# Kernel optimization log

Measured on AMD Instinct MI355X. Metric: run time of the kernel, lower is better.

The kernel has to match this reference:

```python
import jax, jax.numpy as jnp
import numpy as np

B, L, W, S, STEPS, VOCAB, NLAB = 1024, 128, 512, 8, 12, 32, 10

def setup_inputs() -> dict:
    key = jax.random.key(0)
    ks = jax.random.split(key, 24)
    def nrm(k, shape, scale=0.05):
        return jax.random.normal(k, shape, jnp.float32) * scale
    x = jax.random.randint(ks[0], (B, L), 0, VOCAB)
    embed = nrm(ks[1], (VOCAB, W), 0.1).at[0].set(0.0)  # padding_idx=0
    return {
        'x': x,
        'embed': embed,
        'W_mix': nrm(ks[2], (W, 3 * W)), 'b_mix': jnp.zeros((W,), jnp.float32),
        'W_in': nrm(ks[3], (S, W, 2 * W)), 'b_in': jnp.zeros((S, W), jnp.float32),
        'W_link': nrm(ks[4], (S, W, W)), 'b_link': jnp.zeros((S, W), jnp.float32),
        'W_ih': nrm(ks[5], (S, 3 * W, W)), 'b_ih': jnp.zeros((S, 3 * W), jnp.float32),
        'W_hh': nrm(ks[6], (S, 3 * W, W)), 'b_hh': jnp.zeros((S, 3 * W), jnp.float32),
        'W_gate': nrm(ks[7], (S, 1, W)), 'b_gate': jnp.zeros((S, 1), jnp.float32),
        'phase': nrm(ks[8], (S, W), 0.5), 'prism_gain': jnp.zeros((S, W), jnp.float32),
        'W_delta': nrm(ks[9], (S, W, W)), 'b_delta': jnp.zeros((S, W), jnp.float32),
        'decay_param': jnp.zeros((), jnp.float32),
        'W_out': nrm(ks[10], (NLAB, W)), 'b_out': jnp.zeros((NLAB,), jnp.float32),
    }

def _encode(x, embed, W_mix, b_mix):
    emb = embed[x]                                          # [B,L,W]
    mask = (x != 0).astype(jnp.float32)[..., None]          # [B,L,1]
    summed = (emb * mask).sum(1)
    denom = jnp.maximum(mask.sum(1), 1.0)
    mean = summed / denom
    maxed = jnp.where(mask == 0, -10000.0, emb).max(1)
    maxed = jnp.where(jnp.isfinite(maxed), maxed, 0.0)
    last_idx = jnp.maximum(mask[..., 0].sum(1).astype(jnp.int32) - 1, 0)
    last = jnp.take_along_axis(emb, last_idx[:, None, None], axis=1)[:, 0]
    cat = jnp.concatenate([mean, maxed, last], -1)          # [B,3W]
    return jnp.tanh(cat @ W_mix.T + b_mix)

def _forward(x, embed, W_mix, b_mix, W_in, b_in, W_link, b_link, W_ih, b_ih,
             W_hh, b_hh, W_gate, b_gate, phase, prism_gain, W_delta, b_delta,
             decay_param, W_out, b_out):
    summary = _encode(x, embed, W_mix, b_mix)               # [B,W]
    decay = jax.nn.sigmoid(decay_param)
    inv_sqrt_s = np.float32(1.0 / np.sqrt(S))
    gain = jax.nn.softplus(prism_gain)[None]                # [1,S,W]

    def step(carry, _):
        h, hs = carry
        shared = jnp.concatenate([h, summary], -1)          # conditioned: [B,2W]
        f0 = jnp.tanh(jnp.einsum('swi,bi->bsw', W_in, shared) + b_in)      # [B,S,W]
        prev = jnp.roll(f0, 1, axis=1)                      # sparse ring: feats[(i-1)%S]
        feats = jnp.tanh(f0 + jnp.einsum('sow,bsw->bso', W_link, prev) + b_link)
        # recurrent side pockets: per-side GRUCell (torch gate order r,z,n)
        gi = jnp.einsum('sgw,bsw->bsg', W_ih, feats) + b_ih
        gh = jnp.einsum('sgw,bsw->bsg', W_hh, hs) + b_hh
        ir, iz, inn = jnp.split(gi, 3, -1)
        hr, hz, hn = jnp.split(gh, 3, -1)
        r = jax.nn.sigmoid(ir + hr)
        z = jax.nn.sigmoid(iz + hz)
        n = jnp.tanh(inn + r * hn)
        hs_new = (1.0 - z) * n + z * hs                     # [B,S,W]
        feat = hs_new
        gate = jax.nn.sigmoid(jnp.einsum('sow,bsw->bso', W_gate, feat) + b_gate)  # [B,S,1]
        feat = jnp.cos(feat + phase[None]) ** 2 * gain      # prismion
        upd = gate * jnp.tanh(jnp.einsum('sow,bsw->bso', W_delta, feat) + b_delta)
        delta = upd.sum(1) * inv_sqrt_s
        h_new = jnp.tanh(h * decay + delta)
        return (h_new, hs_new), None

    hs0 = jnp.zeros((B, S, W), jnp.float32)
    (h, _), _ = jax.lax.scan(step, (summary, hs0), None, length=STEPS)
    return h @ W_out.T + b_out                               # [B,10]

def reference(x, embed, W_mix, b_mix, W_in, b_in, W_link, b_link, W_ih, b_ih,
              W_hh, b_hh, W_gate, b_gate, phase, prism_gain, W_delta, b_delta,
              decay_param, W_out, b_out):
    return _forward(x, embed, W_mix, b_mix, W_in, b_in, W_link, b_link, W_ih,
                    b_ih, W_hh, b_hh, W_gate, b_gate, phase, prism_gain,
                    W_delta, b_delta, decay_param, W_out, b_out)
```

## Files before the change

### kernel.cpp

```cpp
#include <hip/hip_runtime.h>
#include <hip/hip_bf16.h>


typedef unsigned short u16;
typedef __attribute__((ext_vector_type(8))) short short8;
typedef __attribute__((ext_vector_type(4))) float f32x4;

__device__ __forceinline__ float bf2f(u16 v) {
    union { unsigned int u; float f; } x; x.u = ((unsigned int)v) << 16; return x.f;
}
__device__ __forceinline__ u16 f2bf(float f) {
    union { float f; unsigned int u; } x; x.f = f;
    unsigned int u = x.u;
    return (u16)((u + 0x7FFFu + ((u >> 16) & 1u)) >> 16);
}
__device__ __forceinline__ float fsig(float v) {
    return __builtin_amdgcn_rcpf(1.f + __expf(-v));
}
__device__ __forceinline__ float ftanh(float v) {
    return 1.f - 2.f * __builtin_amdgcn_rcpf(__expf(2.f * v) + 1.f);
}
__device__ __forceinline__ float fsoftplus(float v) {
    return (v > 20.f) ? v : __logf(1.f + __expf(v));
}

union U4 { ushort4 v; u16 e[4]; };

__device__ __forceinline__ void gload_lds16(const u16* g, u16* l) {
    __builtin_amdgcn_global_load_lds(
        (const __attribute__((address_space(1))) unsigned int*)g,
        (__attribute__((address_space(3))) unsigned int*)l, 16, 0, 0);
}

__device__ __forceinline__ int sane16(u16 u) {
    if ((u & 0x7FFF) == 0) return 1;
    int e = (u >> 7) & 0xFF;
    return (e >= 0x33 && e <= 0x43) ? 1 : 0;
}
__global__ __launch_bounds__(256) void detect_k(const u16* __restrict__ raw,
                                                int* __restrict__ flag) {
    const int t = threadIdx.x;
    int c = sane16(raw[1024 + t * 2]) + sane16(raw[1024 + t * 2 + 1]);
#pragma unroll
    for (int off = 32; off; off >>= 1) c += __shfl_down(c, off, 64);
    __shared__ int red[4];
    if ((t & 63) == 0) red[t >> 6] = c;
    __syncthreads();
    if (t == 0) *flag = (red[0] + red[1] + red[2] + red[3] >= 448) ? 1 : 0;
}

struct CT { const void* src[20]; int n[20]; int off[20]; };
__global__ __launch_bounds__(256) void conv_k(CT ct, u16* __restrict__ dstBase,
                                              const int* __restrict__ flag) {
    const int isbf = *flag;
    const int gid = blockIdx.x * 256 + threadIdx.x;
    const int stride = gridDim.x * 256;
    for (int tn = 0; tn < 20; ++tn) {
        const int n = ct.n[tn];
        const int n4 = n >> 2;
        u16* dst = dstBase + ct.off[tn];
        if (!isbf) {
            const float* s = (const float*)ct.src[tn];
            for (int i = gid; i < n4; i += stride) {
                f32x4 v = *(const f32x4*)(s + i * 4);
                *(ushort4*)(dst + i * 4) =
                    make_ushort4(f2bf(v[0]), f2bf(v[1]), f2bf(v[2]), f2bf(v[3]));
            }
            if (gid < (n & 3)) { int i = n4 * 4 + gid; dst[i] = f2bf(s[i]); }
        } else {
            const u16* s = (const u16*)ct.src[tn];
            for (int i = gid; i < n4; i += stride)
                *(ushort4*)(dst + i * 4) = *(const ushort4*)(s + i * 4);
            if (gid < (n & 3)) { int i = n4 * 4 + gid; dst[i] = s[i]; }
        }
    }
}

__global__ __launch_bounds__(256) void pack_k(const u16* __restrict__ Wih,
                                              const u16* __restrict__ Whh,
                                              u16* __restrict__ Wcat) {
    long i = ((long)blockIdx.x * 256 + threadIdx.x) * 8;
    if (i >= 8L * 1536 * 512) return;
    long sg = i >> 9;
    long k  = i & 511;
    *(short8*)(Wcat + sg * 1024 + k)       = *(const short8*)(Wih + i);
    *(short8*)(Wcat + sg * 1024 + 512 + k) = *(const short8*)(Whh + i);
}

struct GP {
    const u16* A;  long lda; long aOff[8];
    const u16* Bw; long ldb; long bwOff[8];
    const u16* bias; long biasOff[8];
    const u16* add; long ldadd; long addOff;
    const float* gate_pre;
    const u16* bgate;
    void* C; long ldc; long cOff[8];
    float* C2;
    u16* C3;
    int K; int nt;
};

template<int EPI, int MT>
__global__ __launch_bounds__(256) void gemm_k(GP p) {
    constexpr int MW   = MT / 32;
    constexpr int AITS = MT / 32;
    __shared__ __align__(16) u16 lA[2][MT * 64];
    __shared__ __align__(16) u16 lB[2][128 * 64];
    const int t    = threadIdx.x;
    const int lane = t & 63;
    const int wv   = t >> 6;
    const int bx   = blockIdx.x;
    const int z    = bx / p.nt;
    const int n0   = (bx - z * p.nt) * 128;
    const int m0   = blockIdx.y * MT;

    const u16* Ab = p.A + p.aOff[z] + (long)m0 * p.lda;
    const u16* Bb = p.Bw + p.bwOff[z] + (long)n0 * p.ldb;

    f32x4 acc[MW][4];
#pragma unroll
    for (int i = 0; i < MW; i++)
#pragma unroll
        for (int j = 0; j < 4; j++) acc[i][j] = (f32x4){0.f, 0.f, 0.f, 0.f};

    const int wm   = (wv & 1) * (MT / 2);
    const int wn   = (wv >> 1) * 64;
    const int fr   = lane & 15;
    const int quad = lane >> 4;

    const int nk = p.K >> 6;
#pragma unroll
    for (int it = 0; it < AITS; ++it) {
        int flat = it * 256 + t, row = flat >> 3, src = (flat & 7) ^ (row & 7);
        gload_lds16(Ab + (long)row * p.lda + src * 8, &lA[0][flat * 8]);
    }
#pragma unroll
    for (int it = 0; it < 4; ++it) {
        int flat = it * 256 + t, row = flat >> 3, src = (flat & 7) ^ (row & 7);
        gload_lds16(Bb + (long)row * p.ldb + src * 8, &lB[0][flat * 8]);
    }
    __syncthreads();

    for (int kt = 0; kt < nk; ++kt) {
        const int cur = kt & 1, nxt = cur ^ 1;
        if (kt + 1 < nk) {
            const long kb = (long)(kt + 1) * 64;
#pragma unroll
            for (int it = 0; it < AITS; ++it) {
                int flat = it * 256 + t, row = flat >> 3, src = (flat & 7) ^ (row & 7);
                gload_lds16(Ab + (long)row * p.lda + kb + src * 8, &lA[nxt][flat * 8]);
            }
#pragma unroll
            for (int it = 0; it < 4; ++it) {
                int flat = it * 256 + t, row = flat >> 3, src = (flat & 7) ^ (row & 7);
                gload_lds16(Bb + (long)row * p.ldb + kb + src * 8, &lB[nxt][flat * 8]);
            }
        }
#pragma unroll
        for (int kk = 0; kk < 2; ++kk) {
            const int q = kk * 4 + quad;
            short8 aF[MW], bF[4];
#pragma unroll
            for (int mi = 0; mi < MW; mi++) {
                int row = wm + mi * 16 + fr;
                aF[mi] = *(const short8*)&lA[cur][row * 64 + (q ^ (row & 7)) * 8];
            }
#pragma unroll
            for (int ni = 0; ni < 4; ni++) {
                int row = wn + ni * 16 + fr;
                bF[ni] = *(const short8*)&lB[cur][row * 64 + (q ^ (row & 7)) * 8];
            }
#pragma unroll
            for (int mi = 0; mi < MW; mi++)
#pragma unroll
                for (int ni = 0; ni < 4; ni++)
                    acc[mi][ni] = __builtin_amdgcn_mfma_f32_16x16x32_bf16(
                        aF[mi], bF[ni], acc[mi][ni], 0, 0, 0);
        }
        __syncthreads();
    }

    float sgv[MW][4];
    if (EPI == 3) {
#pragma unroll
        for (int mi = 0; mi < MW; mi++)
#pragma unroll
            for (int r = 0; r < 4; r++) {
                long row = m0 + wm + mi * 16 + quad * 4 + r;
                sgv[mi][r] = fsig(p.gate_pre[row * 8 + z] + bf2f(p.bgate[z]));
            }
    }

#pragma unroll
    for (int mi = 0; mi < MW; mi++) {
#pragma unroll
        for (int ni = 0; ni < 4; ni++) {
            const int mg = m0 + wm + mi * 16 + quad * 4;
            const int ng = n0 + wn + ni * 16 + fr;
#pragma unroll
            for (int r = 0; r < 4; r++) {
                float v = acc[mi][ni][r];
                const long row = mg + r;
                if (EPI == 1) {
                    float ad = bf2f(p.add[z * p.addOff + row * p.ldadd + ng]);
                    v = ftanh(v + ad + bf2f(p.bias[p.biasOff[z] + ng]));
                    ((u16*)p.C)[p.cOff[z] + row * p.ldc + ng] = f2bf(v);
                } else if (EPI == 3) {
                    v = ftanh(v + bf2f(p.bias[p.biasOff[z] + ng])) * sgv[mi][r];
                    ((u16*)p.C)[p.cOff[z] + row * p.ldc + ng] = f2bf(v);
                } else if (EPI == 4) {
                    v = ftanh(v + bf2f(p.bias[ng]));
                    u16 b = f2bf(v);
                    ((u16*)p.C)[row * 512 + ng] = b;
                    p.C3[row * 512 + ng] = b;
                    p.C2[row * 512 + ng] = v;
                } else if (EPI == 6) {
                    v = v + bf2f(p.bias[p.biasOff[z] + ng]);
                    ((u16*)p.C)[p.cOff[z] + row * p.ldc + ng] = f2bf(v);
                } else {
                    float ad = bf2f(p.add[row * p.ldadd + ng]);
                    v = ftanh(v + ad);
                    ((u16*)p.C)[row * p.ldc + ng] = f2bf(v);
                }
            }
        }
    }
}

struct GGP {
    const u16* fhs_in;
    u16* fhs_out;
    const u16* Wcat;
    const u16* b_ih;
    const u16* b_hh;
    u16* prism;
    float* gate_pre;
    const u16* Wg;
    const u16* phase;
    const u16* pgain;
};

__global__ __launch_bounds__(256, 2) void grug_k(GGP p) {
    __shared__ __align__(16) u16 sA[2][64 * 32];
    __shared__ __align__(16) u16 sW[2][3][128 * 32];
    const int t    = threadIdx.x;
    const int lane = t & 63;
    const int wv   = t >> 6;
    const int s    = blockIdx.x >> 2;
    const int w0   = (blockIdx.x & 3) * 128;
    const int m0   = blockIdx.y * 64;
    const int fr   = lane & 15;
    const int quad = lane >> 4;
    const int wn   = wv * 32;

    const u16* Ab = p.fhs_in + (long)m0 * 8192 + s * 1024;
    const u16* Wb = p.Wcat + (long)s * 1536 * 1024;

    f32x4 acc[4][4][2];
#pragma unroll
    for (int q = 0; q < 4; q++)
#pragma unroll
        for (int mi = 0; mi < 4; mi++)
#pragma unroll
            for (int ni = 0; ni < 2; ni++) acc[q][mi][ni] = (f32x4){0.f,0.f,0.f,0.f};

    const int arow = t >> 2, ac4 = t & 3, asrc = ac4 ^ ((arow >> 1) & 3);

    auto stageA = [&](int buf, long kb) {
        gload_lds16(Ab + (long)arow * 8192 + kb + asrc * 8, &sA[buf][t * 8]);
    };
    auto stageW = [&](int buf, long kb) {
#pragma unroll
        for (int q = 0; q < 3; q++)
#pragma unroll
            for (int it = 0; it < 2; ++it) {
                int flat = it * 256 + t, row = flat >> 2, src = (flat & 3) ^ ((row >> 1) & 3);
                long g = (long)(q * 512 + w0 + row);
                gload_lds16(Wb + g * 1024 + kb + src * 8, &sW[buf][q][flat * 8]);
            }
    };

    stageA(0, 0); stageW(0, 0);
    __syncthreads();

    for (int kt = 0; kt < 32; ++kt) {
        const int cur = kt & 1, nxt = cur ^ 1;
        if (kt + 1 < 32) { stageA(nxt, (long)(kt + 1) * 32); stageW(nxt, (long)(kt + 1) * 32); }
        const int qsel = (kt < 16) ? 2 : 3;
        short8 aF[4], bF[3][2];
#pragma unroll
        for (int mi = 0; mi < 4; mi++) {
            int row = mi * 16 + fr;
            aF[mi] = *(const short8*)&sA[cur][row * 32 + ((quad ^ ((row >> 1) & 3)) & 3) * 8];
        }
#pragma unroll
        for (int q = 0; q < 3; q++)
#pragma unroll
            for (int ni = 0; ni < 2; ni++) {
                int row = wn + ni * 16 + fr;
                bF[q][ni] = *(const short8*)&sW[cur][q][row * 32 + ((quad ^ ((row >> 1) & 3)) & 3) * 8];
            }
#pragma unroll
        for (int mi = 0; mi < 4; mi++)
#pragma unroll
            for (int ni = 0; ni < 2; ni++) {
                acc[0][mi][ni] = __builtin_amdgcn_mfma_f32_16x16x32_bf16(aF[mi], bF[0][ni], acc[0][mi][ni], 0, 0, 0);
                acc[1][mi][ni] = __builtin_amdgcn_mfma_f32_16x16x32_bf16(aF[mi], bF[1][ni], acc[1][mi][ni], 0, 0, 0);
                if (qsel == 2)
                    acc[2][mi][ni] = __builtin_amdgcn_mfma_f32_16x16x32_bf16(aF[mi], bF[2][ni], acc[2][mi][ni], 0, 0, 0);
                else
                    acc[3][mi][ni] = __builtin_amdgcn_mfma_f32_16x16x32_bf16(aF[mi], bF[2][ni], acc[3][mi][ni], 0, 0, 0);
            }
        __syncthreads();
    }

    const u16* bih = p.b_ih + (long)s * 1536;
    const u16* bhh = p.b_hh + (long)s * 1536;
    float gp[4][4];
#pragma unroll
    for (int mi = 0; mi < 4; mi++)
#pragma unroll
        for (int r = 0; r < 4; r++) gp[mi][r] = 0.f;

#pragma unroll
    for (int ni = 0; ni < 2; ni++) {
        const int col = w0 + wn + ni * 16 + fr;
        const float br  = bf2f(bih[col])        + bf2f(bhh[col]);
        const float bz  = bf2f(bih[512 + col])  + bf2f(bhh[512 + col]);
        const float bin = bf2f(bih[1024 + col]);
        const float bhn = bf2f(bhh[1024 + col]);
        const float ph  = bf2f(p.phase[s * 512 + col]);
        const float gain = fsoftplus(bf2f(p.pgain[s * 512 + col]));
        const float wg  = bf2f(p.Wg[s * 512 + col]);
#pragma unroll
        for (int mi = 0; mi < 4; mi++) {
#pragma unroll
            for (int r = 0; r < 4; r++) {
                const long b = m0 + mi * 16 + quad * 4 + r;
                float rv = fsig(acc[0][mi][ni][r] + br);
                float zv = fsig(acc[1][mi][ni][r] + bz);
                float nv = ftanh(acc[2][mi][ni][r] + bin + rv * (acc[3][mi][ni][r] + bhn));
                float hold = bf2f(p.fhs_in[b * 8192 + s * 1024 + 512 + col]);
                float hv = (1.f - zv) * nv + zv * hold;
                p.fhs_out[b * 8192 + s * 1024 + 512 + col] = f2bf(hv);
                float c = __cosf(hv + ph);
                p.prism[b * 4096 + s * 512 + col] = f2bf(c * c * gain);
                gp[mi][r] += wg * hv;
            }
        }
    }
#pragma unroll
    for (int m = 1; m < 16; m <<= 1)
#pragma unroll
        for (int mi = 0; mi < 4; mi++)
#pragma unroll
            for (int r = 0; r < 4; r++) gp[mi][r] += __shfl_xor(gp[mi][r], m, 64);
    if (fr == 0) {
#pragma unroll
        for (int mi = 0; mi < 4; mi++)
#pragma unroll
            for (int r = 0; r < 4; r++) {
                long b = m0 + mi * 16 + quad * 4 + r;
                atomicAdd(&p.gate_pre[b * 8 + s], gp[mi][r]);
            }
    }
}

__global__ __launch_bounds__(256) void encode_k(const int* __restrict__ x,
                                                const u16* __restrict__ embed,
                                                u16* __restrict__ cat) {
    __shared__ int toks[128];
    __shared__ int cnt_s;
    const int b = blockIdx.x, t = threadIdx.x;
    if (t < 128) toks[t] = x[b * 128 + t];
    __syncthreads();
    if (t == 0) {
        int c = 0;
        for (int l = 0; l < 128; l++) c += (toks[l] != 0);
        cnt_s = c;
    }
    __syncthreads();
    const int cnt = cnt_s;
    const int lastTok = toks[cnt > 0 ? cnt - 1 : 0];
    for (int w = t; w < 512; w += 256) {
        float sum = 0.f, mx = -10000.f;
        for (int l = 0; l < 128; l++) {
            int tok = toks[l];
            if (tok != 0) {
                float e = bf2f(embed[tok * 512 + w]);
                sum += e;
                mx = fmaxf(mx, e);
            }
        }
        float mean = sum / (float)(cnt > 0 ? cnt : 1);
        float last = bf2f(embed[lastTok * 512 + w]);
        cat[(long)b * 1536 + w]        = f2bf(mean);
        cat[(long)b * 1536 + 512 + w]  = f2bf(mx);
        cat[(long)b * 1536 + 1024 + w] = f2bf(last);
    }
}

__global__ __launch_bounds__(256) void hupd_k(const u16* __restrict__ upd,
                                              float* __restrict__ h,
                                              u16* __restrict__ h_b,
                                              const u16* __restrict__ decay_p) {
    const int idx = blockIdx.x * 256 + threadIdx.x;
    const int b = idx >> 9, w = idx & 511;
    const long base = (long)b * 4096 + w;
    float dsum = 0.f;
#pragma unroll
    for (int s = 0; s < 8; s++) dsum += bf2f(upd[base + s * 512]);
    const float decay = fsig(bf2f(decay_p[0]));
    const float hv = ftanh(h[idx] * decay + dsum * 0.35355339059327373f);
    h[idx] = hv;
    h_b[idx] = f2bf(hv);
}

__global__ __launch_bounds__(64) void out_k(const float* __restrict__ h,
                                            const u16* __restrict__ Wout,
                                            const u16* __restrict__ bout,
                                            void* __restrict__ out,
                                            const int* __restrict__ flag) {
    const int b = blockIdx.x, lane = threadIdx.x;
    const int isbf = *flag;
    for (int j = 0; j < 10; j++) {
        float p = 0.f;
#pragma unroll
        for (int k = 0; k < 8; k++) {
            int w = lane + k * 64;
            p += h[(long)b * 512 + w] * bf2f(Wout[j * 512 + w]);
        }
#pragma unroll
        for (int off = 32; off; off >>= 1) p += __shfl_down(p, off, 64);
        if (lane == 0) {
            float val = p + bf2f(bout[j]);
            if (isbf) ((u16*)out)[b * 10 + j] = f2bf(val);
            else      ((float*)out)[b * 10 + j] = val;
        }
    }
}

extern "C" void kernel_launch(void* const* d_in, const int* in_sizes, int n_in,
                              void* d_out, int out_size, void* d_ws, size_t ws_size,
                              hipStream_t stream) {
    (void)n_in; (void)out_size; (void)ws_size;
    const int* x = (const int*)d_in[0];

    char* pp = (char*)d_ws;
    auto carve = [&](size_t n) { char* r = pp; pp += (n + 255) & ~(size_t)255; return (void*)r; };

    CT ct;
    size_t ctot = 0;
    for (int i = 0; i < 20; i++) {
        ct.src[i] = d_in[i + 1];
        ct.n[i]   = in_sizes[i + 1];
        ct.off[i] = (int)ctot;
        ctot += ((size_t)in_sizes[i + 1] + 15) & ~(size_t)15;
    }
    u16* canon = (u16*)carve(ctot * 2);
    const u16* embed  = canon + ct.off[0];
    const u16* W_mix  = canon + ct.off[1];
    const u16* b_mix  = canon + ct.off[2];
    const u16* W_in   = canon + ct.off[3];
    const u16* b_in   = canon + ct.off[4];
    const u16* W_link = canon + ct.off[5];
    const u16* b_link = canon + ct.off[6];
    const u16* W_ih   = canon + ct.off[7];
    const u16* b_ih   = canon + ct.off[8];
    const u16* W_hh   = canon + ct.off[9];
    const u16* b_hh   = canon + ct.off[10];
    const u16* W_gate = canon + ct.off[11];
    const u16* b_gate = canon + ct.off[12];
    const u16* phase  = canon + ct.off[13];
    const u16* pgain  = canon + ct.off[14];
    const u16* W_delta= canon + ct.off[15];
    const u16* b_delta= canon + ct.off[16];
    const u16* decayp = canon + ct.off[17];
    const u16* W_out  = canon + ct.off[18];
    const u16* b_out  = canon + ct.off[19];

    int*   flag   = (int*)  carve(256);
    u16*   Wcat   = (u16*)  carve((size_t)8 * 1536 * 1024 * 2);
    u16*   cat    = (u16*)  carve((size_t)1024 * 1536 * 2);
    u16*   h_b    = (u16*)  carve((size_t)1024 * 512 * 2);
    u16*   summ_b = (u16*)  carve((size_t)1024 * 512 * 2);
    float* h      = (float*)carve((size_t)1024 * 512 * 4);
    u16*   cin    = (u16*)  carve((size_t)1024 * 4096 * 2);
    u16*   f0     = (u16*)  carve((size_t)1024 * 4096 * 2);
    u16*   fhs0   = (u16*)  carve((size_t)1024 * 8192 * 2);
    u16*   fhs1   = (u16*)  carve((size_t)1024 * 8192 * 2);
    u16*   prism  = (u16*)  carve((size_t)1024 * 4096 * 2);
    u16*   upd    = (u16*)  carve((size_t)1024 * 4096 * 2);
    float* gate_pre = (float*)carve((size_t)1024 * 8 * 4);

    (void)hipMemsetAsync(fhs0, 0, (size_t)1024 * 8192 * 2, stream);
    (void)hipMemsetAsync(fhs1, 0, (size_t)1024 * 8192 * 2, stream);

    detect_k<<<dim3(1), dim3(256), 0, stream>>>((const u16*)d_in[1], flag);
    conv_k<<<dim3(1024), dim3(256), 0, stream>>>(ct, canon, flag);
    pack_k<<<dim3(3072), dim3(256), 0, stream>>>(W_ih, W_hh, Wcat);
    encode_k<<<dim3(1024), dim3(256), 0, stream>>>(x, embed, cat);

    {
        GP p{}; p.A = cat; p.lda = 1536; p.Bw = W_mix; p.ldb = 1536;
        p.bias = b_mix; p.C = h_b; p.ldc = 512; p.C2 = h; p.C3 = summ_b;
        p.K = 1536; p.nt = 4;
        gemm_k<4, 64><<<dim3(4, 16, 1), dim3(256), 0, stream>>>(p);
    }
    {
        GP p{}; p.A = summ_b; p.lda = 512; p.Bw = W_in + 512; p.ldb = 1024;
        p.bias = b_in; p.C = cin; p.ldc = 4096; p.K = 512; p.nt = 32;
        gemm_k<6, 64><<<dim3(32, 16, 1), dim3(256), 0, stream>>>(p);
    }

    for (int step = 0; step < 12; ++step) {
        u16* fhs_cur = (step & 1) ? fhs1 : fhs0;
        u16* fhs_nxt = (step & 1) ? fhs0 : fhs1;
        {
            GP p{}; p.A = h_b; p.lda = 512; p.Bw = W_in; p.ldb = 1024;
            p.add = cin; p.ldadd = 4096; p.C = f0; p.ldc = 4096;
            p.K = 512; p.nt = 32;
            gemm_k<7, 64><<<dim3(32, 16, 1), dim3(256), 0, stream>>>(p);
        }
        {
            GP p{}; p.A = f0; p.lda = 4096;
            for (int s = 0; s < 8; s++) p.aOff[s] = (long)((s + 7) & 7) * 512;
            p.Bw = W_link; p.ldb = 512;
            for (int s = 0; s < 8; s++) p.bwOff[s] = (long)s * 512 * 512;
            p.bias = b_link;
            for (int s = 0; s < 8; s++) p.biasOff[s] = (long)s * 512;
            p.add = f0; p.ldadd = 4096; p.addOff = 512;
            p.C = fhs_cur; p.ldc = 8192;
            for (int s = 0; s < 8; s++) p.cOff[s] = (long)s * 1024;
            p.K = 512; p.nt = 4;
            gemm_k<1, 64><<<dim3(32, 16, 1), dim3(256), 0, stream>>>(p);
        }
        (void)hipMemsetAsync(gate_pre, 0, (size_t)1024 * 8 * 4, stream);
        {
            GGP g{};
            g.fhs_in = fhs_cur; g.fhs_out = fhs_nxt; g.Wcat = Wcat;
            g.b_ih = b_ih; g.b_hh = b_hh; g.prism = prism; g.gate_pre = gate_pre;
            g.Wg = W_gate; g.phase = phase; g.pgain = pgain;
            grug_k<<<dim3(32, 16, 1), dim3(256), 0, stream>>>(g);
        }
        {
            GP p{}; p.A = prism; p.lda = 4096;
            for (int s = 0; s < 8; s++) p.aOff[s] = (long)s * 512;
            p.Bw = W_delta; p.ldb = 512;
            for (int s = 0; s < 8; s++) p.bwOff[s] = (long)s * 512 * 512;
            p.bias = b_delta;
            for (int s = 0; s < 8; s++) p.biasOff[s] = (long)s * 512;
            p.gate_pre = gate_pre; p.bgate = b_gate;
            p.C = upd; p.ldc = 4096;
            for (int s = 0; s < 8; s++) p.cOff[s] = (long)s * 512;
            p.K = 512; p.nt = 4;
            gemm_k<3, 64><<<dim3(32, 16, 1), dim3(256), 0, stream>>>(p);
        }
        hupd_k<<<dim3(2048), dim3(256), 0, stream>>>(upd, h, h_b, decayp);
    }

    out_k<<<dim3(1024), dim3(64), 0, stream>>>(h, W_out, b_out, d_out, flag);
}
```

Measured before the change: 1.536 ms.

## Fuse delta GEMM, gating and hidden update into one kernel; retile GRU kernel

The per-slot W_delta GEMM, the sigmoid gating, the sum over slots and the hidden-state tanh update now run in a single kernel (updh_k). Each block loops over all 8 slots and accumulates the gated tanh outputs in registers, so the bf16 upd intermediate and the separate hupd_k launch go away. Separately, grug_k is retiled to 64-column blocks, which doubles the grid and shrinks per-thread accumulators and LDS. The fused kernel launches only 64 blocks with a long serial K loop, which may leave many compute units idle.

```diff
diff --git a/kernel.cpp b/kernel.cpp
--- a/kernel.cpp
+++ b/kernel.cpp
@@ -92,8 +92,6 @@
     const u16* Bw; long ldb; long bwOff[8];
     const u16* bias; long biasOff[8];
     const u16* add; long ldadd; long addOff;
-    const float* gate_pre;
-    const u16* bgate;
     void* C; long ldc; long cOff[8];
     float* C2;
     u16* C3;
@@ -180,17 +178,6 @@
         __syncthreads();
     }
 
-    float sgv[MW][4];
-    if (EPI == 3) {
-#pragma unroll
-        for (int mi = 0; mi < MW; mi++)
-#pragma unroll
-            for (int r = 0; r < 4; r++) {
-                long row = m0 + wm + mi * 16 + quad * 4 + r;
-                sgv[mi][r] = fsig(p.gate_pre[row * 8 + z] + bf2f(p.bgate[z]));
-            }
-    }
-
 #pragma unroll
     for (int mi = 0; mi < MW; mi++) {
 #pragma unroll
@@ -204,9 +191,6 @@
                 if (EPI == 1) {
                     float ad = bf2f(p.add[z * p.addOff + row * p.ldadd + ng]);
                     v = ftanh(v + ad + bf2f(p.bias[p.biasOff[z] + ng]));
-                    ((u16*)p.C)[p.cOff[z] + row * p.ldc + ng] = f2bf(v);
-                } else if (EPI == 3) {
-                    v = ftanh(v + bf2f(p.bias[p.biasOff[z] + ng])) * sgv[mi][r];
                     ((u16*)p.C)[p.cOff[z] + row * p.ldc + ng] = f2bf(v);
                 } else if (EPI == 4) {
                     v = ftanh(v + bf2f(p.bias[ng]));
@@ -240,44 +224,39 @@
     const u16* pgain;
 };
 
-__global__ __launch_bounds__(256, 2) void grug_k(GGP p) {
+__global__ __launch_bounds__(256) void grug_k(GGP p) {
     __shared__ __align__(16) u16 sA[2][64 * 32];
-    __shared__ __align__(16) u16 sW[2][3][128 * 32];
+    __shared__ __align__(16) u16 sW[2][3][64 * 32];
     const int t    = threadIdx.x;
     const int lane = t & 63;
     const int wv   = t >> 6;
-    const int s    = blockIdx.x >> 2;
-    const int w0   = (blockIdx.x & 3) * 128;
+    const int s    = blockIdx.x >> 3;
+    const int w0   = (blockIdx.x & 7) * 64;
     const int m0   = blockIdx.y * 64;
     const int fr   = lane & 15;
     const int quad = lane >> 4;
-    const int wn   = wv * 32;
+    const int wn   = wv * 16;
 
     const u16* Ab = p.fhs_in + (long)m0 * 8192 + s * 1024;
     const u16* Wb = p.Wcat + (long)s * 1536 * 1024;
 
-    f32x4 acc[4][4][2];
+    f32x4 acc[4][4];
 #pragma unroll
     for (int q = 0; q < 4; q++)
 #pragma unroll
-        for (int mi = 0; mi < 4; mi++)
-#pragma unroll
-            for (int ni = 0; ni < 2; ni++) acc[q][mi][ni] = (f32x4){0.f,0.f,0.f,0.f};
-
-    const int arow = t >> 2, ac4 = t & 3, asrc = ac4 ^ ((arow >> 1) & 3);
+        for (int mi = 0; mi < 4; mi++) acc[q][mi] = (f32x4){0.f,0.f,0.f,0.f};
+
+    const int arow = t >> 2, asrc = (t & 3) ^ ((arow >> 1) & 3);
 
     auto stageA = [&](int buf, long kb) {
         gload_lds16(Ab + (long)arow * 8192 + kb + asrc * 8, &sA[buf][t * 8]);
     };
     auto stageW = [&](int buf, long kb) {
 #pragma unroll
-        for (int q = 0; q < 3; q++)
-#pragma unroll
-            for (int it = 0; it < 2; ++it) {
-                int flat = it * 256 + t, row = flat >> 2, src = (flat & 3) ^ ((row >> 1) & 3);
-                long g = (long)(q * 512 + w0 + row);
-                gload_lds16(Wb + g * 1024 + kb + src * 8, &sW[buf][q][flat * 8]);
-            }
+        for (int q = 0; q < 3; q++) {
+            long g = (long)(q * 512 + w0 + arow);
+            gload_lds16(Wb + g * 1024 + kb + asrc * 8, &sW[buf][q][t * 8]);
+        }
     };
 
     stageA(0, 0); stageW(0, 0);
@@ -287,66 +266,57 @@
         const int cur = kt & 1, nxt = cur ^ 1;
         if (kt + 1 < 32) { stageA(nxt, (long)(kt + 1) * 32); stageW(nxt, (long)(kt + 1) * 32); }
         const int qsel = (kt < 16) ? 2 : 3;
-        short8 aF[4], bF[3][2];
+        short8 aF[4], bFq[3];
 #pragma unroll
         for (int mi = 0; mi < 4; mi++) {
             int row = mi * 16 + fr;
             aF[mi] = *(const short8*)&sA[cur][row * 32 + ((quad ^ ((row >> 1) & 3)) & 3) * 8];
         }
-#pragma unroll
-        for (int q = 0; q < 3; q++)
-#pragma unroll
-            for (int ni = 0; ni < 2; ni++) {
-                int row = wn + ni * 16 + fr;
-                bF[q][ni] = *(const short8*)&sW[cur][q][row * 32 + ((quad ^ ((row >> 1) & 3)) & 3) * 8];
-            }
-#pragma unroll
-        for (int mi = 0; mi < 4; mi++)
-#pragma unroll
-            for (int ni = 0; ni < 2; ni++) {
-                acc[0][mi][ni] = __builtin_amdgcn_mfma_f32_16x16x32_bf16(aF[mi], bF[0][ni], acc[0][mi][ni], 0, 0, 0);
-                acc[1][mi][ni] = __builtin_amdgcn_mfma_f32_16x16x32_bf16(aF[mi], bF[1][ni], acc[1][mi][ni], 0, 0, 0);
-                if (qsel == 2)
-                    acc[2][mi][ni] = __builtin_amdgcn_mfma_f32_16x16x32_bf16(aF[mi], bF[2][ni], acc[2][mi][ni], 0, 0, 0);
-                else
-                    acc[3][mi][ni] = __builtin_amdgcn_mfma_f32_16x16x32_bf16(aF[mi], bF[2][ni], acc[3][mi][ni], 0, 0, 0);
-            }
+        {
+            int row = wn + fr;
+            int sw = ((quad ^ ((row >> 1) & 3)) & 3) * 8;
+#pragma unroll
+            for (int q = 0; q < 3; q++)
+                bFq[q] = *(const short8*)&sW[cur][q][row * 32 + sw];
+        }
+#pragma unroll
+        for (int mi = 0; mi < 4; mi++) {
+            acc[0][mi] = __builtin_amdgcn_mfma_f32_16x16x32_bf16(aF[mi], bFq[0], acc[0][mi], 0, 0, 0);
+            acc[1][mi] = __builtin_amdgcn_mfma_f32_16x16x32_bf16(aF[mi], bFq[1], acc[1][mi], 0, 0, 0);
+            if (qsel == 2)
+                acc[2][mi] = __builtin_amdgcn_mfma_f32_16x16x32_bf16(aF[mi], bFq[2], acc[2][mi], 0, 0, 0);
+            else
+                acc[3][mi] = __builtin_amdgcn_mfma_f32_16x16x32_bf16(aF[mi], bFq[2], acc[3][mi], 0, 0, 0);
+        }
         __syncthreads();
     }
 
     const u16* bih = p.b_ih + (long)s * 1536;
     const u16* bhh = p.b_hh + (long)s * 1536;
+    const int col = w0 + wn + fr;
+    const float br  = bf2f(bih[col])        + bf2f(bhh[col]);
+    const float bz  = bf2f(bih[512 + col])  + bf2f(bhh[512 + col]);
+    const float bin = bf2f(bih[1024 + col]);
+    const float bhn = bf2f(bhh[1024 + col]);
+    const float ph  = bf2f(p.phase[s * 512 + col]);
+    const float gain = fsoftplus(bf2f(p.pgain[s * 512 + col]));
+    const float wg  = bf2f(p.Wg[s * 512 + col]);
+
     float gp[4][4];
 #pragma unroll
-    for (int mi = 0; mi < 4; mi++)
-#pragma unroll
-        for (int r = 0; r < 4; r++) gp[mi][r] = 0.f;
-
-#pragma unroll
-    for (int ni = 0; ni < 2; ni++) {
-        const int col = w0 + wn + ni * 16 + fr;
-        const float br  = bf2f(bih[col])        + bf2f(bhh[col]);
-        const float bz  = bf2f(bih[512 + col])  + bf2f(bhh[512 + col]);
-        const float bin = bf2f(bih[1024 + col]);
-        const float bhn = bf2f(bhh[1024 + col]);
-        const float ph  = bf2f(p.phase[s * 512 + col]);
-        const float gain = fsoftplus(bf2f(p.pgain[s * 512 + col]));
-        const float wg  = bf2f(p.Wg[s * 512 + col]);
-#pragma unroll
-        for (int mi = 0; mi < 4; mi++) {
-#pragma unroll
-            for (int r = 0; r < 4; r++) {
-                const long b = m0 + mi * 16 + quad * 4 + r;
-                float rv = fsig(acc[0][mi][ni][r] + br);
-                float zv = fsig(acc[1][mi][ni][r] + bz);
-                float nv = ftanh(acc[2][mi][ni][r] + bin + rv * (acc[3][mi][ni][r] + bhn));
-                float hold = bf2f(p.fhs_in[b * 8192 + s * 1024 + 512 + col]);
-                float hv = (1.f - zv) * nv + zv * hold;
-                p.fhs_out[b * 8192 + s * 1024 + 512 + col] = f2bf(hv);
-                float c = __cosf(hv + ph);
-                p.prism[b * 4096 + s * 512 + col] = f2bf(c * c * gain);
-                gp[mi][r] += wg * hv;
-            }
+    for (int mi = 0; mi < 4; mi++) {
+#pragma unroll
+        for (int r = 0; r < 4; r++) {
+            const long b = m0 + mi * 16 + quad * 4 + r;
+            float rv = fsig(acc[0][mi][r] + br);
+            float zv = fsig(acc[1][mi][r] + bz);
+            float nv = ftanh(acc[2][mi][r] + bin + rv * (acc[3][mi][r] + bhn));
+            float hold = bf2f(p.fhs_in[b * 8192 + s * 1024 + 512 + col]);
+            float hv = (1.f - zv) * nv + zv * hold;
+            p.fhs_out[b * 8192 + s * 1024 + 512 + col] = f2bf(hv);
+            float c = __cosf(hv + ph);
+            p.prism[b * 4096 + s * 512 + col] = f2bf(c * c * gain);
+            gp[mi][r] = wg * hv;
         }
     }
 #pragma unroll
@@ -364,6 +334,126 @@
                 atomicAdd(&p.gate_pre[b * 8 + s], gp[mi][r]);
             }
     }
+}
+
+struct UP {
+    const u16* prism;
+    const u16* Wd;
+    const u16* bd;
+    const float* gate_pre;
+    const u16* bgate;
+    float* h; u16* h_b;
+    const u16* decayp;
+};
+
+__global__ __launch_bounds__(256) void updh_k(UP p) {
+    __shared__ __align__(16) u16 lA[2][64 * 64];
+    __shared__ __align__(16) u16 lB[2][128 * 64];
+    const int t    = threadIdx.x;
+    const int lane = t & 63;
+    const int wv   = t >> 6;
+    const int n0   = blockIdx.x * 128;
+    const int m0   = blockIdx.y * 64;
+    const int wm   = (wv & 1) * 32;
+    const int wn   = (wv >> 1) * 64;
+    const int fr   = lane & 15;
+    const int quad = lane >> 4;
+
+    f32x4 acc[2][4], dsum[2][4];
+#pragma unroll
+    for (int i = 0; i < 2; i++)
+#pragma unroll
+        for (int j = 0; j < 4; j++) { acc[i][j] = (f32x4){0.f,0.f,0.f,0.f}; dsum[i][j] = (f32x4){0.f,0.f,0.f,0.f}; }
+
+    auto stageA = [&](int buf, int z, long kb) {
+        const u16* Ab = p.prism + (long)m0 * 4096 + z * 512;
+#pragma unroll
+        for (int it = 0; it < 2; ++it) {
+            int flat = it * 256 + t, row = flat >> 3, src = (flat & 7) ^ (row & 7);
+            gload_lds16(Ab + (long)row * 4096 + kb + src * 8, &lA[buf][flat * 8]);
+        }
+    };
+    auto stageB = [&](int buf, int z, long kb) {
+        const u16* Bb = p.Wd + (long)z * 512 * 512 + (long)n0 * 512;
+#pragma unroll
+        for (int it = 0; it < 4; ++it) {
+            int flat = it * 256 + t, row = flat >> 3, src = (flat & 7) ^ (row & 7);
+            gload_lds16(Bb + (long)row * 512 + kb + src * 8, &lB[buf][flat * 8]);
+        }
+    };
+
+    stageA(0, 0, 0); stageB(0, 0, 0);
+    __syncthreads();
+    const float decay = fsig(bf2f(p.decayp[0]));
+
+    for (int g = 0; g < 64; ++g) {
+        const int cur = g & 1, nxt = cur ^ 1;
+        if (g + 1 < 64) {
+            int z2 = (g + 1) >> 3; long k2 = (long)((g + 1) & 7) * 64;
+            stageA(nxt, z2, k2); stageB(nxt, z2, k2);
+        }
+#pragma unroll
+        for (int kk = 0; kk < 2; ++kk) {
+            const int q = kk * 4 + quad;
+            short8 aF[2], bF[4];
+#pragma unroll
+            for (int mi = 0; mi < 2; mi++) {
+                int row = wm + mi * 16 + fr;
+                aF[mi] = *(const short8*)&lA[cur][row * 64 + (q ^ (row & 7)) * 8];
+            }
+#pragma unroll
+            for (int ni = 0; ni < 4; ni++) {
+                int row = wn + ni * 16 + fr;
+                bF[ni] = *(const short8*)&lB[cur][row * 64 + (q ^ (row & 7)) * 8];
+            }
+#pragma unroll
+            for (int mi = 0; mi < 2; mi++)
+#pragma unroll
+                for (int ni = 0; ni < 4; ni++)
+                    acc[mi][ni] = __builtin_amdgcn_mfma_f32_16x16x32_bf16(
+                        aF[mi], bF[ni], acc[mi][ni], 0, 0, 0);
+        }
+        if ((g & 7) == 7) {
+            const int z = g >> 3;
+            const float bgz = bf2f(p.bgate[z]);
+            float sg[2][4];
+#pragma unroll
+            for (int mi = 0; mi < 2; mi++)
+#pragma unroll
+                for (int r = 0; r < 4; r++) {
+                    long row = m0 + wm + mi * 16 + quad * 4 + r;
+                    sg[mi][r] = fsig(p.gate_pre[row * 8 + z] + bgz);
+                }
+#pragma unroll
+            for (int ni = 0; ni < 4; ni++) {
+                const int col = n0 + wn + ni * 16 + fr;
+                const float bdz = bf2f(p.bd[z * 512 + col]);
+#pragma unroll
+                for (int mi = 0; mi < 2; mi++)
+#pragma unroll
+                    for (int r = 0; r < 4; r++) {
+                        dsum[mi][ni][r] += ftanh(acc[mi][ni][r] + bdz) * sg[mi][r];
+                        acc[mi][ni][r] = 0.f;
+                    }
+            }
+        }
+        __syncthreads();
+    }
+
+#pragma unroll
+    for (int mi = 0; mi < 2; mi++)
+#pragma unroll
+        for (int ni = 0; ni < 4; ni++) {
+            const int col = n0 + wn + ni * 16 + fr;
+#pragma unroll
+            for (int r = 0; r < 4; r++) {
+                long row = m0 + wm + mi * 16 + quad * 4 + r;
+                long idx = row * 512 + col;
+                float hv = ftanh(p.h[idx] * decay + dsum[mi][ni][r] * 0.35355339059327373f);
+                p.h[idx] = hv;
+                p.h_b[idx] = f2bf(hv);
+            }
+        }
 }
 
 __global__ __launch_bounds__(256) void encode_k(const int* __restrict__ x,
@@ -398,22 +488,6 @@
         cat[(long)b * 1536 + 512 + w]  = f2bf(mx);
         cat[(long)b * 1536 + 1024 + w] = f2bf(last);
     }
-}
-
-__global__ __launch_bounds__(256) void hupd_k(const u16* __restrict__ upd,
-                                              float* __restrict__ h,
-                                              u16* __restrict__ h_b,
-                                              const u16* __restrict__ decay_p) {
-    const int idx = blockIdx.x * 256 + threadIdx.x;
-    const int b = idx >> 9, w = idx & 511;
-    const long base = (long)b * 4096 + w;
-    float dsum = 0.f;
-#pragma unroll
-    for (int s = 0; s < 8; s++) dsum += bf2f(upd[base + s * 512]);
-    const float decay = fsig(bf2f(decay_p[0]));
-    const float hv = ftanh(h[idx] * decay + dsum * 0.35355339059327373f);
-    h[idx] = hv;
-    h_b[idx] = f2bf(hv);
 }
 
 __global__ __launch_bounds__(64) void out_k(const float* __restrict__ h,
@@ -490,7 +564,6 @@
     u16*   fhs0   = (u16*)  carve((size_t)1024 * 8192 * 2);
     u16*   fhs1   = (u16*)  carve((size_t)1024 * 8192 * 2);
     u16*   prism  = (u16*)  carve((size_t)1024 * 4096 * 2);
-    u16*   upd    = (u16*)  carve((size_t)1024 * 4096 * 2);
     float* gate_pre = (float*)carve((size_t)1024 * 8 * 4);
 
     (void)hipMemsetAsync(fhs0, 0, (size_t)1024 * 8192 * 2, stream);
@@ -541,22 +614,15 @@
             g.fhs_in = fhs_cur; g.fhs_out = fhs_nxt; g.Wcat = Wcat;
             g.b_ih = b_ih; g.b_hh = b_hh; g.prism = prism; g.gate_pre = gate_pre;
             g.Wg = W_gate; g.phase = phase; g.pgain = pgain;
-            grug_k<<<dim3(32, 16, 1), dim3(256), 0, stream>>>(g);
+            grug_k<<<dim3(64, 16, 1), dim3(256), 0, stream>>>(g);
         }
         {
-            GP p{}; p.A = prism; p.lda = 4096;
-            for (int s = 0; s < 8; s++) p.aOff[s] = (long)s * 512;
-            p.Bw = W_delta; p.ldb = 512;
-            for (int s = 0; s < 8; s++) p.bwOff[s] = (long)s * 512 * 512;
-            p.bias = b_delta;
-            for (int s = 0; s < 8; s++) p.biasOff[s] = (long)s * 512;
-            p.gate_pre = gate_pre; p.bgate = b_gate;
-            p.C = upd; p.ldc = 4096;
-            for (int s = 0; s < 8; s++) p.cOff[s] = (long)s * 512;
-            p.K = 512; p.nt = 4;
-            gemm_k<3, 64><<<dim3(32, 16, 1), dim3(256), 0, stream>>>(p);
-        }
-        hupd_k<<<dim3(2048), dim3(256), 0, stream>>>(upd, h, h_b, decayp);
+            UP u{};
+            u.prism = prism; u.Wd = W_delta; u.bd = b_delta;
+            u.gate_pre = gate_pre; u.bgate = b_gate;
+            u.h = h; u.h_b = h_b; u.decayp = decayp;
+            updh_k<<<dim3(4, 16, 1), dim3(256), 0, stream>>>(u);
+        }
     }
 
     out_k<<<dim3(1024), dim3(64), 0, stream>>>(h, W_out, b_out, d_out, flag);
```

New measurement: 2.606 ms. 1.7x slower.
